# Kernel tuning notes

Measured on AMD Instinct MI355X. Metric: run time of the kernel, lower is better.

Reference implementation:

```python
import jax, jax.numpy as jnp
import numpy as np

B, R, IN_DIM = 32, 512, 1024
K, D = 4096, 256  # num_codebook_vectors, latent_dim
OUT_DIM = 1024
BETA = 0.25


def setup_inputs() -> dict:
    key = jax.random.key(0)
    ks = jax.random.split(key, 5)
    scale = 1.0 / K
    return {
        "z": jax.random.normal(ks[0], (B, R, IN_DIM), dtype=jnp.float32),
        "W_qa": jax.random.normal(ks[1], (IN_DIM, 2 * D), dtype=jnp.float32) * (IN_DIM ** -0.5),
        "b_qa": jnp.zeros((2 * D,), dtype=jnp.float32),
        "emb1": jax.random.uniform(ks[2], (K, D), dtype=jnp.float32, minval=-scale, maxval=scale),
        "emb2": jax.random.uniform(ks[3], (K, D), dtype=jnp.float32, minval=-scale, maxval=scale),
        "W_pq": jax.random.normal(ks[4], (2 * D, OUT_DIM), dtype=jnp.float32) * ((2 * D) ** -0.5),
        "b_pq": jnp.zeros((OUT_DIM,), dtype=jnp.float32),
    }


def _vq(z_h, emb):
    # z_h: [B, R, D], emb: [K, D]
    zf = z_h.reshape(-1, D)  # [N, D]
    # squared-distance matrix via GEMM: [N, K]
    d = (jnp.sum(zf * zf, axis=1, keepdims=True)
         + jnp.sum(emb * emb, axis=1)
         - 2.0 * zf @ emb.T)
    idx = jnp.argmin(d, axis=1)  # [N]
    z_q = emb[idx].reshape(z_h.shape)  # gather [B, R, D]
    enc_loss = jnp.mean((jax.lax.stop_gradient(z_q) - z_h) ** 2, axis=-1)
    code_loss = jnp.mean((z_q - jax.lax.stop_gradient(z_h)) ** 2, axis=-1)
    loss = enc_loss + BETA * code_loss  # [B, R]
    z_q_st = z_h + jax.lax.stop_gradient(z_q - z_h)  # straight-through
    return z_q_st, idx.reshape(z_h.shape[:2]), loss


def reference(z, W_qa, b_qa, emb1, emb2, W_pq, b_pq):
    h = z @ W_qa + b_qa  # [B, R, 2D]
    z1, z2 = h[..., :D], h[..., D:]
    zq1, idx1, loss1 = _vq(z1, emb1)
    zq2, idx2, loss2 = _vq(z2, emb2)
    loss = 0.5 * (loss1 + loss2)  # [B, R]
    z_q = jnp.concatenate([zq1, zq2], axis=-1) @ W_pq + b_pq  # [B, R, OUT_DIM]
    return z_q, idx1, idx2, loss
```

## Files before the change

### kernel.cpp

```cpp
#include <hip/hip_runtime.h>
#include <cstdint>
#include <cstddef>

#define MROWS 16384
#define INDIM 1024
#define DD    256
#define TWO_D 512
#define KC    4096
#define OUTD  1024
#define NZQ   (MROWS * OUTD)

typedef short bfrag __attribute__((ext_vector_type(8)));
typedef float ffrag __attribute__((ext_vector_type(4)));

__device__ __forceinline__ ushort f2bf(float f) {
    uint u = __float_as_uint(f);
    return (ushort)((u + 0x7FFFu + ((u >> 16) & 1u)) >> 16);
}

#define GLD16(dst, src)                                                        \
    __builtin_amdgcn_global_load_lds(                                          \
        (const __attribute__((address_space(1))) unsigned int*)(src),          \
        (__attribute__((address_space(3))) unsigned int*)(dst), 16, 0, 0)

__global__ __launch_bounds__(256) void k_gemm1(const float* __restrict__ z,
                                               const float* __restrict__ Wqa,
                                               const float* __restrict__ bqa,
                                               float* __restrict__ h,
                                               ushort* __restrict__ hbf) {
    __shared__ float As[2][128][16];
    __shared__ float Bs[2][16][128];
    const int tid = threadIdx.x;
    const int l = tid & 63, w = tid >> 6;
    const int tx = tid & 15, ty = tid >> 4;
    const int rb = blockIdx.x * 128;
    const int cb = blockIdx.y * 128;

    float acc[8][8] = {};

    const int sA = 4 * ((l & 3) ^ ((l >> 4) & 3));
    const float* aA0 = z + (size_t)(rb + 32 * w + (l >> 2)) * INDIM + sA;
    const float* aA1 = aA0 + (size_t)16 * INDIM;
    const float* bB0 = Wqa + (size_t)(4 * w + (l >> 5)) * TWO_D + cb + (l & 31) * 4;
    const float* bB1 = bB0 + (size_t)2 * TWO_D;

#define STAGE(buf, k0)                                                         \
    do {                                                                       \
        GLD16(&As[buf][32 * w][0],      aA0 + (k0));                           \
        GLD16(&As[buf][32 * w + 16][0], aA1 + (k0));                           \
        GLD16(&Bs[buf][4 * w][0],       bB0 + (size_t)(k0) * TWO_D);           \
        GLD16(&Bs[buf][4 * w + 2][0],   bB1 + (size_t)(k0) * TWO_D);           \
    } while (0)

    STAGE(0, 0);
    __syncthreads();

    const int xk = ty & 3;
    for (int t = 0; t < 64; ++t) {
        const int cur = t & 1;
        if (t < 63) STAGE(cur ^ 1, (t + 1) * 16);
        #pragma unroll
        for (int q = 0; q < 4; ++q) {
            float fa[8][4];
            #pragma unroll
            for (int i = 0; i < 4; ++i) {
                *reinterpret_cast<float4*>(&fa[i][0]) =
                    *reinterpret_cast<const float4*>(&As[cur][ty * 4 + i][(q ^ xk) * 4]);
                *reinterpret_cast<float4*>(&fa[4 + i][0]) =
                    *reinterpret_cast<const float4*>(&As[cur][64 + ty * 4 + i][(q ^ xk) * 4]);
            }
            #pragma unroll
            for (int c = 0; c < 4; ++c) {
                const int kk = q * 4 + c;
                float4 b0 = *reinterpret_cast<const float4*>(&Bs[cur][kk][tx * 4]);
                float4 b1 = *reinterpret_cast<const float4*>(&Bs[cur][kk][64 + tx * 4]);
                float bv[8] = {b0.x, b0.y, b0.z, b0.w, b1.x, b1.y, b1.z, b1.w};
                #pragma unroll
                for (int i = 0; i < 8; ++i)
                    #pragma unroll
                    for (int j = 0; j < 8; ++j)
                        acc[i][j] = fmaf(fa[i][c], bv[j], acc[i][j]);
            }
        }
        __syncthreads();
    }
#undef STAGE

    #pragma unroll
    for (int i = 0; i < 8; ++i) {
        const int row = rb + ((i < 4) ? (ty * 4 + i) : (64 + ty * 4 + i - 4));
        #pragma unroll
        for (int jh = 0; jh < 2; ++jh) {
            const int col = cb + jh * 64 + tx * 4;
            float v0 = acc[i][jh * 4 + 0] + bqa[col + 0];
            float v1 = acc[i][jh * 4 + 1] + bqa[col + 1];
            float v2 = acc[i][jh * 4 + 2] + bqa[col + 2];
            float v3 = acc[i][jh * 4 + 3] + bqa[col + 3];
            float4 vf = {v0, v1, v2, v3};
            *reinterpret_cast<float4*>(&h[(size_t)row * TWO_D + col]) = vf;
            ushort u[4] = {f2bf(v0), f2bf(v1), f2bf(v2), f2bf(v3)};
            *reinterpret_cast<uint2*>(&hbf[(size_t)row * TWO_D + col]) =
                *reinterpret_cast<uint2*>(u);
        }
    }
}

__global__ __launch_bounds__(256) void k_rnorm(const float* __restrict__ h,
                                               float* __restrict__ Rn) {
    const int wave = threadIdx.x >> 6;
    const int lane = threadIdx.x & 63;
    const int item = blockIdx.x * 4 + wave;
    const int row  = item & (MROWS - 1);
    const int half = item >> 14;
    float4 v = *reinterpret_cast<const float4*>(&h[(size_t)row * TWO_D + half * DD + lane * 4]);
    float s = v.x * v.x + v.y * v.y + v.z * v.z + v.w * v.w;
    #pragma unroll
    for (int off = 32; off; off >>= 1) s += __shfl_down(s, off, 64);
    if (lane == 0) Rn[half * MROWS + row] = s;
}

__global__ __launch_bounds__(256) void k_cvt(const float* __restrict__ e1,
                                             const float* __restrict__ e2,
                                             const float* __restrict__ Wpq,
                                             ushort* __restrict__ ebf,
                                             ushort* __restrict__ wbfT) {
    const int b = blockIdx.x;
    if (b < 2048) {
        const size_t v = ((size_t)b * 256 + threadIdx.x) * 4;
        const size_t half = (size_t)KC * DD;
        const float* src = (v < half) ? (e1 + v) : (e2 + (v - half));
        float4 f = *reinterpret_cast<const float4*>(src);
        ebf[v + 0] = f2bf(f.x); ebf[v + 1] = f2bf(f.y);
        ebf[v + 2] = f2bf(f.z); ebf[v + 3] = f2bf(f.w);
    } else {
        const int e = ((b - 2048) * 256 + threadIdx.x) * 4;
        const int k = e >> 10, c = e & 1023;
        float4 f = *reinterpret_cast<const float4*>(&Wpq[e]);
        wbfT[(size_t)(c + 0) * TWO_D + k] = f2bf(f.x);
        wbfT[(size_t)(c + 1) * TWO_D + k] = f2bf(f.y);
        wbfT[(size_t)(c + 2) * TWO_D + k] = f2bf(f.z);
        wbfT[(size_t)(c + 3) * TWO_D + k] = f2bf(f.w);
    }
}

__global__ __launch_bounds__(256) void k_score_mfma(const ushort* __restrict__ hbf,
                                                    const ushort* __restrict__ ebf,
                                                    uint* __restrict__ cand) {
    __shared__ ushort Ab[2][4][128][8];
    __shared__ ushort Bb[2][4][128][8];
    const int tid = threadIdx.x;
    const int l = tid & 63, w = tid >> 6;
    const int rb    = blockIdx.x * 128;
    const int cbcol = blockIdx.y * 128;
    const int cbk   = blockIdx.z;
    const ushort* hb = hbf + cbk * DD;
    const ushort* eb = ebf + (size_t)cbk * KC * DD;

    const int ry = (w & 1) * 64;
    const int cy = (w >> 1) * 64;

    const int koct = (w ^ ((l >> 1) & 3)) * 8;
    const ushort* aS0 = hb + (size_t)(rb + l) * TWO_D + koct;
    const ushort* aS1 = hb + (size_t)(rb + 64 + l) * TWO_D + koct;
    const ushort* bS0 = eb + (size_t)(cbcol + l) * DD + koct;
    const ushort* bS1 = eb + (size_t)(cbcol + 64 + l) * DD + koct;

#define SSTAGE(buf, k0)                                                        \
    do {                                                                       \
        GLD16(&Ab[buf][w][0][0],  aS0 + (k0));                                 \
        GLD16(&Ab[buf][w][64][0], aS1 + (k0));                                 \
        GLD16(&Bb[buf][w][0][0],  bS0 + (k0));                                 \
        GLD16(&Bb[buf][w][64][0], bS1 + (k0));                                 \
    } while (0)

    ffrag acc[4][4];
    #pragma unroll
    for (int i = 0; i < 4; ++i)
        #pragma unroll
        for (int j = 0; j < 4; ++j)
            acc[i][j] = (ffrag){0.f, 0.f, 0.f, 0.f};

    SSTAGE(0, 0);
    __syncthreads();

    const int q = l >> 4, li = l & 15;
    for (int c = 0; c < 8; ++c) {
        const int cur = c & 1;
        if (c < 7) SSTAGE(cur ^ 1, (c + 1) * 32);
        bfrag afr[4], bfr[4];
        #pragma unroll
        for (int rf = 0; rf < 4; ++rf) {
            const int r = ry + rf * 16 + li;
            afr[rf] = *reinterpret_cast<const bfrag*>(&Ab[cur][q ^ ((r >> 1) & 3)][r][0]);
        }
        #pragma unroll
        for (int cf = 0; cf < 4; ++cf) {
            const int cc = cy + cf * 16 + li;
            bfr[cf] = *reinterpret_cast<const bfrag*>(&Bb[cur][q ^ ((cc >> 1) & 3)][cc][0]);
        }
        #pragma unroll
        for (int rf = 0; rf < 4; ++rf)
            #pragma unroll
            for (int cf = 0; cf < 4; ++cf)
                acc[rf][cf] = __builtin_amdgcn_mfma_f32_16x16x32_bf16(afr[rf], bfr[cf],
                                                                      acc[rf][cf], 0, 0, 0);
        __syncthreads();
    }
#undef SSTAGE

    const int seg = blockIdx.y * 2 + (w >> 1);
    #pragma unroll
    for (int rf = 0; rf < 4; ++rf) {
        #pragma unroll
        for (int reg = 0; reg < 4; ++reg) {
            const int row = rb + ry + rf * 16 + q * 4 + reg;
            uint k1 = 0, k2 = 0;
            #pragma unroll
            for (int cf = 0; cf < 4; ++cf) {
                float v = acc[rf][cf][reg];
                const int code = cbcol + cy + cf * 16 + li;
                uint u = __float_as_uint(v);
                u ^= (0x80000000u | (uint)((int)u >> 31));
                const uint key = (u & 0xFFFFF000u) | (uint)code;
                if (key > k1) { k2 = k1; k1 = key; }
                else if (key > k2) { k2 = key; }
            }
            #pragma unroll
            for (int m = 1; m < 16; m <<= 1) {
                uint o1 = __shfl_xor((int)k1, m, 64);
                uint o2 = __shfl_xor((int)k2, m, 64);
                uint n1 = k1 > o1 ? k1 : o1;
                uint lo = k1 > o1 ? o1 : k1;
                uint hi2 = k2 > o2 ? k2 : o2;
                k2 = lo > hi2 ? lo : hi2;
                k1 = n1;
            }
            if (li == 0) {
                const size_t base = ((size_t)cbk * MROWS + row) * 128 + seg * 2;
                cand[base] = k1; cand[base + 1] = k2;
            }
        }
    }
}

__global__ __launch_bounds__(256) void k_reduce(const uint* __restrict__ cand,
                                                const float* __restrict__ h,
                                                const float* __restrict__ emb1,
                                                const float* __restrict__ emb2,
                                                const float* __restrict__ Rn,
                                                float* __restrict__ dout_idx) {
    const int tid = threadIdx.x;
    const int l = tid & 63, w = tid >> 6;
    const int g = l & 7;
    const int item = blockIdx.x * 32 + w * 8 + (l >> 3);
    const int cb  = item >> 14;
    const int row = item & (MROWS - 1);

    const uint* kp = cand + (size_t)item * 128 + g * 16;
    uint k[16];
    #pragma unroll
    for (int j = 0; j < 4; ++j) {
        uint4 v = *reinterpret_cast<const uint4*>(kp + j * 4);
        k[j * 4 + 0] = v.x; k[j * 4 + 1] = v.y;
        k[j * 4 + 2] = v.z; k[j * 4 + 3] = v.w;
    }

    uint mykey = 0;
    #pragma unroll
    for (int t = 0; t < 8; ++t) {
        uint m = k[0];
        #pragma unroll
        for (int j = 1; j < 16; ++j) m = k[j] > m ? k[j] : m;
        #pragma unroll
        for (int off = 1; off < 8; off <<= 1) {
            uint o = (uint)__shfl_xor((int)m, off, 64);
            m = o > m ? o : m;
        }
        #pragma unroll
        for (int j = 0; j < 16; ++j) k[j] = (k[j] == m) ? 0u : k[j];
        if (g == t) mykey = m;
    }

    const int code = (int)(mykey & 0xFFFu);
    const float* hr = h + (size_t)row * TWO_D + cb * DD;
    const float* er = (cb ? emb2 : emb1) + (size_t)code * DD;
    float M = 0.f;
    for (int d = 0; d < DD; d += 4) {
        float4 a = *reinterpret_cast<const float4*>(hr + d);
        float4 b = *reinterpret_cast<const float4*>(er + d);
        M = fmaf(a.x, b.x, M); M = fmaf(a.y, b.y, M);
        M = fmaf(a.z, b.z, M); M = fmaf(a.w, b.w, M);
    }
    float dd = Rn[cb * MROWS + row] - 2.0f * M;
    int c2 = code;
    #pragma unroll
    for (int off = 1; off < 8; off <<= 1) {
        float od = __shfl_xor(dd, off, 64);
        int   oc = __shfl_xor(c2, off, 64);
        if (od < dd || (od == dd && oc < c2)) { dd = od; c2 = oc; }
    }
    if (g == 0) dout_idx[cb * MROWS + row] = (float)c2;
}

__global__ __launch_bounds__(256) void k_loss(const float* __restrict__ h,
                                              const float* __restrict__ emb1,
                                              const float* __restrict__ emb2,
                                              const float* __restrict__ idxf,
                                              float* __restrict__ dout_loss) {
    __shared__ float red[4];
    const int r = blockIdx.x;
    const int d = threadIdx.x;
    const int ia = (int)idxf[r];
    const int ib = (int)idxf[MROWS + r];
    float e1 = emb1[(size_t)ia * DD + d];
    float e2 = emb2[(size_t)ib * DD + d];
    float h1 = h[(size_t)r * TWO_D + d];
    float h2 = h[(size_t)r * TWO_D + DD + d];
    float d1 = e1 - h1, d2 = e2 - h2;
    float p = d1 * d1 + d2 * d2;
    #pragma unroll
    for (int off = 32; off; off >>= 1) p += __shfl_down(p, off, 64);
    const int lane = d & 63, wv = d >> 6;
    if (lane == 0) red[wv] = p;
    __syncthreads();
    if (d == 0) {
        float s = red[0] + red[1] + red[2] + red[3];
        dout_loss[r] = s * (0.625f / 256.0f);
    }
}

__global__ __launch_bounds__(256) void k_gemm2m(const ushort* __restrict__ ebf,
                                                const ushort* __restrict__ wbfT,
                                                const float* __restrict__ idxf,
                                                const float* __restrict__ bpq,
                                                float* __restrict__ out) {
    __shared__ ushort Ab[2][4][128][8];
    __shared__ ushort Bb[2][4][128][8];
    const int tid = threadIdx.x;
    const int l = tid & 63, w = tid >> 6;
    const int rb    = blockIdx.x * 128;
    const int cbcol = blockIdx.y * 128;
    const int ry = (w & 1) * 64;
    const int cy = (w >> 1) * 64;
    const ushort* e1 = ebf;
    const ushort* e2 = ebf + (size_t)KC * DD;

    const int ia0 = (int)idxf[rb + l];
    const int ia1 = (int)idxf[rb + 64 + l];
    const int ib0 = (int)idxf[MROWS + rb + l];
    const int ib1 = (int)idxf[MROWS + rb + 64 + l];

    const int koct = (w ^ ((l >> 1) & 3)) * 8;
    const ushort* aA0 = e1 + (size_t)ia0 * DD + koct;
    const ushort* aA1 = e1 + (size_t)ia1 * DD + koct;
    const ushort* aB0 = e2 + (size_t)ib0 * DD + koct;
    const ushort* aB1 = e2 + (size_t)ib1 * DD + koct;
    const ushort* bS0 = wbfT + (size_t)(cbcol + l) * TWO_D + koct;
    const ushort* bS1 = wbfT + (size_t)(cbcol + 64 + l) * TWO_D + koct;

#define GSTAGE(buf, c)                                                         \
    do {                                                                       \
        const int cbs_ = (c) >> 3;                                             \
        const int ka_  = ((c) * 32) & 255;                                     \
        GLD16(&Ab[buf][w][0][0],  (cbs_ ? aB0 : aA0) + ka_);                   \
        GLD16(&Ab[buf][w][64][0], (cbs_ ? aB1 : aA1) + ka_);                   \
        GLD16(&Bb[buf][w][0][0],  bS0 + (c) * 32);                             \
        GLD16(&Bb[buf][w][64][0], bS1 + (c) * 32);                             \
    } while (0)

    ffrag acc[4][4];
    #pragma unroll
    for (int i = 0; i < 4; ++i)
        #pragma unroll
        for (int j = 0; j < 4; ++j)
            acc[i][j] = (ffrag){0.f, 0.f, 0.f, 0.f};

    GSTAGE(0, 0);
    __syncthreads();

    const int q = l >> 4, li = l & 15;
    for (int c = 0; c < 16; ++c) {
        const int cur = c & 1;
        if (c < 15) GSTAGE(cur ^ 1, c + 1);
        bfrag afr[4], bfr[4];
        #pragma unroll
        for (int rf = 0; rf < 4; ++rf) {
            const int r = ry + rf * 16 + li;
            afr[rf] = *reinterpret_cast<const bfrag*>(&Ab[cur][q ^ ((r >> 1) & 3)][r][0]);
        }
        #pragma unroll
        for (int cf = 0; cf < 4; ++cf) {
            const int cc = cy + cf * 16 + li;
            bfr[cf] = *reinterpret_cast<const bfrag*>(&Bb[cur][q ^ ((cc >> 1) & 3)][cc][0]);
        }
        #pragma unroll
        for (int rf = 0; rf < 4; ++rf)
            #pragma unroll
            for (int cf = 0; cf < 4; ++cf)
                acc[rf][cf] = __builtin_amdgcn_mfma_f32_16x16x32_bf16(afr[rf], bfr[cf],
                                                                      acc[rf][cf], 0, 0, 0);
        __syncthreads();
    }
#undef GSTAGE

    #pragma unroll
    for (int rf = 0; rf < 4; ++rf) {
        #pragma unroll
        for (int reg = 0; reg < 4; ++reg) {
            const int row = rb + ry + rf * 16 + q * 4 + reg;
            #pragma unroll
            for (int cf = 0; cf < 4; ++cf) {
                const int col = cbcol + cy + cf * 16 + li;
                out[(size_t)row * OUTD + col] = acc[rf][cf][reg] + bpq[col];
            }
        }
    }
}

extern "C" void kernel_launch(void* const* d_in, const int* in_sizes, int n_in,
                              void* d_out, int out_size, void* d_ws, size_t ws_size,
                              hipStream_t stream) {
    const float* z    = (const float*)d_in[0];
    const float* Wqa  = (const float*)d_in[1];
    const float* bqa  = (const float*)d_in[2];
    const float* emb1 = (const float*)d_in[3];
    const float* emb2 = (const float*)d_in[4];
    const float* Wpq  = (const float*)d_in[5];
    const float* bpq  = (const float*)d_in[6];
    float* out = (float*)d_out;

    const size_t H = (size_t)MROWS * TWO_D;
    float*  hbuf = (float*)d_ws;
    float*  Rn   = hbuf + H;
    ushort* hbf  = (ushort*)(Rn + 2 * MROWS);
    ushort* ebf  = hbf + H;
    ushort* wbfT = ebf + 2 * (size_t)KC * DD;
    uint*   cand = (uint*)(wbfT + (size_t)OUTD * TWO_D);

    float* dout_idx  = out + NZQ;
    float* dout_loss = out + NZQ + 2 * MROWS;

    k_gemm1<<<dim3(128, 4), 256, 0, stream>>>(z, Wqa, bqa, hbuf, hbf);
    k_rnorm<<<8192, 256, 0, stream>>>(hbuf, Rn);
    k_cvt<<<2560, 256, 0, stream>>>(emb1, emb2, Wpq, ebf, wbfT);
    k_score_mfma<<<dim3(128, 32, 2), 256, 0, stream>>>(hbf, ebf, cand);
    k_reduce<<<1024, 256, 0, stream>>>(cand, hbuf, emb1, emb2, Rn, dout_idx);
    k_loss<<<16384, 256, 0, stream>>>(hbuf, emb1, emb2, dout_idx, dout_loss);
    k_gemm2m<<<dim3(128, 8), 256, 0, stream>>>(ebf, wbfT, dout_idx, bpq, out);
}
```

Measured before the change: 543.1 us.

## Fuse row norms and conversion into GEMM1, compute loss from argmin distances

The separate row-norm and bf16-conversion kernels are folded into the first GEMM launch: extra blocks do the codebook and weight conversion, and the GEMM epilogue writes per-column-block partial row norms. Codebook squared norms are computed during conversion so the reduce kernel can emit the per-row VQ loss as min distance plus code norm. This replaces the gather-based loss kernel with a tiny elementwise combine. It removes two launches and a reread of h and the embeddings, but the loss now comes from the expanded-distance formula, which risks cancellation error relative to the direct difference.

```diff
diff --git a/kernel.cpp b/kernel.cpp
--- a/kernel.cpp
+++ b/kernel.cpp
@@ -23,18 +23,52 @@
         (const __attribute__((address_space(1))) unsigned int*)(src),          \
         (__attribute__((address_space(3))) unsigned int*)(dst), 16, 0, 0)
 
-__global__ __launch_bounds__(256) void k_gemm1(const float* __restrict__ z,
+__global__ __launch_bounds__(256) void k_g1cvt(const float* __restrict__ z,
                                                const float* __restrict__ Wqa,
                                                const float* __restrict__ bqa,
+                                               const float* __restrict__ e1,
+                                               const float* __restrict__ e2,
+                                               const float* __restrict__ Wpq,
                                                float* __restrict__ h,
-                                               ushort* __restrict__ hbf) {
+                                               ushort* __restrict__ hbf,
+                                               ushort* __restrict__ ebf,
+                                               ushort* __restrict__ wbfT,
+                                               float* __restrict__ Rnp,
+                                               float* __restrict__ Ren) {
     __shared__ float As[2][128][16];
     __shared__ float Bs[2][16][128];
+    const int bx = blockIdx.x, by = blockIdx.y;
     const int tid = threadIdx.x;
+
+    if (bx >= 128) {
+        const int b = (bx - 128) * 4 + by;
+        if (b < 2048) {
+            const size_t v = ((size_t)b * 256 + tid) * 4;
+            const size_t half = (size_t)KC * DD;
+            const float* src = (v < half) ? (e1 + v) : (e2 + (v - half));
+            float4 f = *reinterpret_cast<const float4*>(src);
+            ebf[v + 0] = f2bf(f.x); ebf[v + 1] = f2bf(f.y);
+            ebf[v + 2] = f2bf(f.z); ebf[v + 3] = f2bf(f.w);
+            float ss = f.x * f.x + f.y * f.y + f.z * f.z + f.w * f.w;
+            #pragma unroll
+            for (int off = 32; off; off >>= 1) ss += __shfl_down(ss, off, 64);
+            if ((tid & 63) == 0) Ren[b * 4 + (tid >> 6)] = ss;
+        } else {
+            const int e = ((b - 2048) * 256 + tid) * 4;
+            const int k = e >> 10, c = e & 1023;
+            float4 f = *reinterpret_cast<const float4*>(&Wpq[e]);
+            wbfT[(size_t)(c + 0) * TWO_D + k] = f2bf(f.x);
+            wbfT[(size_t)(c + 1) * TWO_D + k] = f2bf(f.y);
+            wbfT[(size_t)(c + 2) * TWO_D + k] = f2bf(f.z);
+            wbfT[(size_t)(c + 3) * TWO_D + k] = f2bf(f.w);
+        }
+        return;
+    }
+
     const int l = tid & 63, w = tid >> 6;
     const int tx = tid & 15, ty = tid >> 4;
-    const int rb = blockIdx.x * 128;
-    const int cb = blockIdx.y * 128;
+    const int rb = bx * 128;
+    const int cb = by * 128;
 
     float acc[8][8] = {};
 
@@ -89,6 +123,7 @@
     #pragma unroll
     for (int i = 0; i < 8; ++i) {
         const int row = rb + ((i < 4) ? (ty * 4 + i) : (64 + ty * 4 + i - 4));
+        float rsum = 0.f;
         #pragma unroll
         for (int jh = 0; jh < 2; ++jh) {
             const int col = cb + jh * 64 + tx * 4;
@@ -101,45 +136,11 @@
             ushort u[4] = {f2bf(v0), f2bf(v1), f2bf(v2), f2bf(v3)};
             *reinterpret_cast<uint2*>(&hbf[(size_t)row * TWO_D + col]) =
                 *reinterpret_cast<uint2*>(u);
-        }
-    }
-}
-
-__global__ __launch_bounds__(256) void k_rnorm(const float* __restrict__ h,
-                                               float* __restrict__ Rn) {
-    const int wave = threadIdx.x >> 6;
-    const int lane = threadIdx.x & 63;
-    const int item = blockIdx.x * 4 + wave;
-    const int row  = item & (MROWS - 1);
-    const int half = item >> 14;
-    float4 v = *reinterpret_cast<const float4*>(&h[(size_t)row * TWO_D + half * DD + lane * 4]);
-    float s = v.x * v.x + v.y * v.y + v.z * v.z + v.w * v.w;
-    #pragma unroll
-    for (int off = 32; off; off >>= 1) s += __shfl_down(s, off, 64);
-    if (lane == 0) Rn[half * MROWS + row] = s;
-}
-
-__global__ __launch_bounds__(256) void k_cvt(const float* __restrict__ e1,
-                                             const float* __restrict__ e2,
-                                             const float* __restrict__ Wpq,
-                                             ushort* __restrict__ ebf,
-                                             ushort* __restrict__ wbfT) {
-    const int b = blockIdx.x;
-    if (b < 2048) {
-        const size_t v = ((size_t)b * 256 + threadIdx.x) * 4;
-        const size_t half = (size_t)KC * DD;
-        const float* src = (v < half) ? (e1 + v) : (e2 + (v - half));
-        float4 f = *reinterpret_cast<const float4*>(src);
-        ebf[v + 0] = f2bf(f.x); ebf[v + 1] = f2bf(f.y);
-        ebf[v + 2] = f2bf(f.z); ebf[v + 3] = f2bf(f.w);
-    } else {
-        const int e = ((b - 2048) * 256 + threadIdx.x) * 4;
-        const int k = e >> 10, c = e & 1023;
-        float4 f = *reinterpret_cast<const float4*>(&Wpq[e]);
-        wbfT[(size_t)(c + 0) * TWO_D + k] = f2bf(f.x);
-        wbfT[(size_t)(c + 1) * TWO_D + k] = f2bf(f.y);
-        wbfT[(size_t)(c + 2) * TWO_D + k] = f2bf(f.z);
-        wbfT[(size_t)(c + 3) * TWO_D + k] = f2bf(f.w);
+            rsum += v0 * v0 + v1 * v1 + v2 * v2 + v3 * v3;
+        }
+        #pragma unroll
+        for (int off = 1; off < 16; off <<= 1) rsum += __shfl_xor(rsum, off, 16);
+        if (tx == 0) Rnp[(size_t)by * MROWS + row] = rsum;
     }
 }
 
@@ -247,8 +248,10 @@
                                                 const float* __restrict__ h,
                                                 const float* __restrict__ emb1,
                                                 const float* __restrict__ emb2,
-                                                const float* __restrict__ Rn,
-                                                float* __restrict__ dout_idx) {
+                                                const float* __restrict__ Rnp,
+                                                const float* __restrict__ Ren,
+                                                float* __restrict__ dout_idx,
+                                                float* __restrict__ lossb) {
     const int tid = threadIdx.x;
     const int l = tid & 63, w = tid >> 6;
     const int g = l & 7;
@@ -291,7 +294,9 @@
         M = fmaf(a.x, b.x, M); M = fmaf(a.y, b.y, M);
         M = fmaf(a.z, b.z, M); M = fmaf(a.w, b.w, M);
     }
-    float dd = Rn[cb * MROWS + row] - 2.0f * M;
+    const float Rn = Rnp[(size_t)(2 * cb) * MROWS + row] +
+                     Rnp[(size_t)(2 * cb + 1) * MROWS + row];
+    float dd = Rn - 2.0f * M;
     int c2 = code;
     #pragma unroll
     for (int off = 1; off < 8; off <<= 1) {
@@ -299,34 +304,16 @@
         int   oc = __shfl_xor(c2, off, 64);
         if (od < dd || (od == dd && oc < c2)) { dd = od; c2 = oc; }
     }
-    if (g == 0) dout_idx[cb * MROWS + row] = (float)c2;
-}
-
-__global__ __launch_bounds__(256) void k_loss(const float* __restrict__ h,
-                                              const float* __restrict__ emb1,
-                                              const float* __restrict__ emb2,
-                                              const float* __restrict__ idxf,
-                                              float* __restrict__ dout_loss) {
-    __shared__ float red[4];
-    const int r = blockIdx.x;
-    const int d = threadIdx.x;
-    const int ia = (int)idxf[r];
-    const int ib = (int)idxf[MROWS + r];
-    float e1 = emb1[(size_t)ia * DD + d];
-    float e2 = emb2[(size_t)ib * DD + d];
-    float h1 = h[(size_t)r * TWO_D + d];
-    float h2 = h[(size_t)r * TWO_D + DD + d];
-    float d1 = e1 - h1, d2 = e2 - h2;
-    float p = d1 * d1 + d2 * d2;
-    #pragma unroll
-    for (int off = 32; off; off >>= 1) p += __shfl_down(p, off, 64);
-    const int lane = d & 63, wv = d >> 6;
-    if (lane == 0) red[wv] = p;
-    __syncthreads();
-    if (d == 0) {
-        float s = red[0] + red[1] + red[2] + red[3];
-        dout_loss[r] = s * (0.625f / 256.0f);
-    }
+    if (g == 0) {
+        dout_idx[cb * MROWS + row] = (float)c2;
+        lossb[cb * MROWS + row] = dd + Ren[cb * KC + c2];
+    }
+}
+
+__global__ __launch_bounds__(256) void k_loss2(const float* __restrict__ lossb,
+                                               float* __restrict__ dout_loss) {
+    const int r = blockIdx.x * 256 + threadIdx.x;
+    dout_loss[r] = (lossb[r] + lossb[MROWS + r]) * (0.625f / 256.0f);
 }
 
 __global__ __launch_bounds__(256) void k_gemm2m(const ushort* __restrict__ ebf,
@@ -430,21 +417,23 @@
     float* out = (float*)d_out;
 
     const size_t H = (size_t)MROWS * TWO_D;
-    float*  hbuf = (float*)d_ws;
-    float*  Rn   = hbuf + H;
-    ushort* hbf  = (ushort*)(Rn + 2 * MROWS);
-    ushort* ebf  = hbf + H;
-    ushort* wbfT = ebf + 2 * (size_t)KC * DD;
-    uint*   cand = (uint*)(wbfT + (size_t)OUTD * TWO_D);
+    float*  hbuf  = (float*)d_ws;
+    float*  Rnp   = hbuf + H;
+    float*  lossb = Rnp + 4 * MROWS;
+    float*  Ren   = lossb + 2 * MROWS;
+    ushort* hbf   = (ushort*)(Ren + 2 * KC);
+    ushort* ebf   = hbf + H;
+    ushort* wbfT  = ebf + 2 * (size_t)KC * DD;
+    uint*   cand  = (uint*)(wbfT + (size_t)OUTD * TWO_D);
 
     float* dout_idx  = out + NZQ;
     float* dout_loss = out + NZQ + 2 * MROWS;
 
-    k_gemm1<<<dim3(128, 4), 256, 0, stream>>>(z, Wqa, bqa, hbuf, hbf);
-    k_rnorm<<<8192, 256, 0, stream>>>(hbuf, Rn);
-    k_cvt<<<2560, 256, 0, stream>>>(emb1, emb2, Wpq, ebf, wbfT);
+    k_g1cvt<<<dim3(768, 4), 256, 0, stream>>>(z, Wqa, bqa, emb1, emb2, Wpq,
+                                              hbuf, hbf, ebf, wbfT, Rnp, Ren);
     k_score_mfma<<<dim3(128, 32, 2), 256, 0, stream>>>(hbf, ebf, cand);
-    k_reduce<<<1024, 256, 0, stream>>>(cand, hbuf, emb1, emb2, Rn, dout_idx);
-    k_loss<<<16384, 256, 0, stream>>>(hbuf, emb1, emb2, dout_idx, dout_loss);
+    k_reduce<<<1024, 256, 0, stream>>>(cand, hbuf, emb1, emb2, Rnp, Ren,
+                                       dout_idx, lossb);
+    k_loss2<<<64, 256, 0, stream>>>(lossb, dout_loss);
     k_gemm2m<<<dim3(128, 8), 256, 0, stream>>>(ebf, wbfT, dout_idx, bpq, out);
 }
```

New measurement: 557.5 us. 2.6% more time.
